# Optimization experiments

Measured on AMD Instinct MI355X. Metric: run time of the kernel, lower is better.

Reference implementation:

```python
import jax, jax.numpy as jnp
import numpy as np
import math

B, N = 1, 512
C_S, C_Z, C_H, H, PQ, PV = 384, 128, 16, 12, 4, 8
INF, EPS = 100000.0, 1e-8


def setup_inputs() -> dict:
    key = jax.random.key(0)
    ks = jax.random.split(key, 16)
    sc = 0.02
    return {
        "s": jax.random.normal(ks[0], (B, N, C_S), jnp.float32),
        "z": jax.random.normal(ks[1], (B, N, N, C_Z), jnp.float32),
        "t_trans": jax.random.normal(ks[2], (B, N, 3), jnp.float32),
        "t_rots": jax.random.normal(ks[3], (B, N, 3, 3), jnp.float32),
        "mask": jnp.ones((B, N), jnp.float32),
        "Wq": jax.random.normal(ks[4], (C_S, H * C_H), jnp.float32) * sc,
        "bq": jnp.zeros((H * C_H,), jnp.float32),
        "Wkv": jax.random.normal(ks[5], (C_S, 2 * H * C_H), jnp.float32) * sc,
        "bkv": jnp.zeros((2 * H * C_H,), jnp.float32),
        "Wqp": jax.random.normal(ks[6], (C_S, H * PQ * 3), jnp.float32) * sc,
        "bqp": jnp.zeros((H * PQ * 3,), jnp.float32),
        "Wkvp": jax.random.normal(ks[7], (C_S, H * (PQ + PV) * 3), jnp.float32) * sc,
        "bkvp": jnp.zeros((H * (PQ + PV) * 3,), jnp.float32),
        "Wb": jax.random.normal(ks[8], (C_Z, H), jnp.float32) * sc,
        "bb": jnp.zeros((H,), jnp.float32),
        "head_weights": jnp.full((H,), 0.5413, jnp.float32),  # softplus^-1(1) init
        "Wout": jax.random.normal(ks[9], (H * (C_Z + C_H + PV * 4), C_S), jnp.float32) * sc,
        "bout": jnp.zeros((C_S,), jnp.float32),
    }


def _split3_stack(x):
    # torch.split into 3 chunks along -1, then stack on new last axis -> [..., P, 3]
    return jnp.stack(jnp.split(x, 3, axis=-1), axis=-1)


def reference(s, z, t_trans, t_rots, mask, Wq, bq, Wkv, bkv, Wqp, bqp, Wkvp, bkvp,
              Wb, bb, head_weights, Wout, bout):
    q = (s @ Wq + bq).reshape(B, N, H, C_H)
    kv = (s @ Wkv + bkv).reshape(B, N, H, 2 * C_H)
    k, v = kv[..., :C_H], kv[..., C_H:]

    # point projections, moved to global frame: r @ p + t
    qp = _split3_stack(s @ Wqp + bqp)                      # [B,N,H*PQ,3] local
    qp = jnp.einsum('bnij,bnpj->bnpi', t_rots, qp) + t_trans[:, :, None, :]
    q_pts = qp.reshape(B, N, H, PQ, 3)
    kvp = _split3_stack(s @ Wkvp + bkvp)                   # [B,N,H*(PQ+PV),3]
    kvp = jnp.einsum('bnij,bnpj->bnpi', t_rots, kvp) + t_trans[:, :, None, :]
    kvp = kvp.reshape(B, N, H, PQ + PV, 3)
    k_pts, v_pts = kvp[..., :PQ, :], kvp[..., PQ:, :]

    b = z @ Wb + bb                                        # [B,N,N,H]

    a = jnp.einsum('bihc,bjhc->bhij', q, k) * math.sqrt(1.0 / (3 * C_H))
    a = a + math.sqrt(1.0 / 3) * jnp.transpose(b, (0, 3, 1, 2))

    # point-distance attention: [B,N,N,H,PQ]
    d2 = jnp.sum((q_pts[:, :, None] - k_pts[:, None]) ** 2, axis=-1)
    hw = jax.nn.softplus(head_weights) * math.sqrt(1.0 / (3 * (PQ * 9.0 / 2)))
    a = a + (-0.5) * jnp.einsum('bijhp,h->bhij', d2, hw)

    square_mask = INF * (mask[:, :, None] * mask[:, None, :] - 1.0)  # [B,N,N]
    a = jax.nn.softmax(a + square_mask[:, None], axis=-1)  # [B,H,N,N]

    o = jnp.einsum('bhij,bjhc->bihc', a, v).reshape(B, N, H * C_H)

    o_pt = jnp.einsum('bhij,bjhpx->bihpx', a, v_pts)       # [B,N,H,PV,3] global
    # invert frame: r^T @ (p - t)
    o_pt = jnp.einsum('bnji,bnhpj->bnhpi', t_rots, o_pt - t_trans[:, :, None, None, :])
    o_pt_norm = jnp.sqrt(jnp.sum(o_pt ** 2, axis=-1) + EPS).reshape(B, N, H * PV)
    o_pt = o_pt.reshape(B, N, H * PV, 3)

    o_pair = jnp.einsum('bhij,bijc->bihc', a, z).reshape(B, N, H * C_Z)

    cat = jnp.concatenate(
        [o, o_pt[..., 0], o_pt[..., 1], o_pt[..., 2], o_pt_norm, o_pair], axis=-1)
    return cat @ Wout + bout
```

## Files before the change

### kernel.cpp

```cpp
#include <hip/hip_runtime.h>
#include <math.h>

#define N 512
#define CS 384
#define CZ 128
#define CH 16
#define NH 12
#define PQ 4
#define PV 8

#define OFF_Q     0
#define OFF_K     98304
#define OFF_QRAW  294912
#define OFF_KVRAW 368640
#define OFF_QPTS  589824
#define OFF_KPTS  663552
#define OFF_VPX   737280
#define OFF_VPY   786432
#define OFF_VPZ   835584
#define OFF_A     884736
#define OFF_CAT   4030464
#define OFF_VT    5111808
#define OFF_WBT   5210112

__global__ __launch_bounds__(384) void init_out_kernel(
    const float* __restrict__ bout, const float* __restrict__ Wb,
    float* __restrict__ out, float* __restrict__ ws)
{
    out[(size_t)blockIdx.x * 384 + threadIdx.x] = bout[threadIdx.x];
    if (blockIdx.x == 0) {
        for (int idx = threadIdx.x; idx < NH * CZ; idx += 384) {
            int h = idx >> 7, c = idx & 127;
            ws[OFF_WBT + idx] = Wb[c * NH + h];
        }
    }
}

__global__ __launch_bounds__(256) void proj_kernel(
    const float* __restrict__ s,
    const float* __restrict__ Wq,  const float* __restrict__ bq,
    const float* __restrict__ Wkv, const float* __restrict__ bkv,
    const float* __restrict__ Wqp, const float* __restrict__ bqp,
    const float* __restrict__ Wkvp,const float* __restrict__ bkvp,
    float* __restrict__ ws)
{
    __shared__ float st[16 * CS];
    const int n0 = blockIdx.x * 16;
    for (int idx = threadIdx.x * 4; idx < 16 * CS; idx += 1024)
        *(float4*)&st[idx] = *(const float4*)&s[n0 * CS + idx];
    __syncthreads();

    const int tc = threadIdx.x & 31;
    const int tr = threadIdx.x >> 5;
    const int u0 = blockIdx.y * 128 + tc * 4;
    const int r0 = tr * 2;

    const float* W; const float* bptr; int ncol, lc0;
    if (u0 < 192)      { W = Wq;   bptr = bq;   ncol = 192; lc0 = u0; }
    else if (u0 < 576) { W = Wkv;  bptr = bkv;  ncol = 384; lc0 = u0 - 192; }
    else if (u0 < 720) { W = Wqp;  bptr = bqp;  ncol = 144; lc0 = u0 - 576; }
    else               { W = Wkvp; bptr = bkvp; ncol = 432; lc0 = u0 - 720; }

    float acc[2][4];
    #pragma unroll
    for (int r = 0; r < 2; r++)
        #pragma unroll
        for (int c = 0; c < 4; c++) acc[r][c] = 0.f;

    for (int k = 0; k < CS; k += 4) {
        float4 w0 = *(const float4*)&W[(k + 0) * ncol + lc0];
        float4 w1 = *(const float4*)&W[(k + 1) * ncol + lc0];
        float4 w2 = *(const float4*)&W[(k + 2) * ncol + lc0];
        float4 w3 = *(const float4*)&W[(k + 3) * ncol + lc0];
        #pragma unroll
        for (int r = 0; r < 2; r++) {
            float4 sv = *(const float4*)&st[(r0 + r) * CS + k];
            acc[r][0] += sv.x * w0.x + sv.y * w1.x + sv.z * w2.x + sv.w * w3.x;
            acc[r][1] += sv.x * w0.y + sv.y * w1.y + sv.z * w2.y + sv.w * w3.y;
            acc[r][2] += sv.x * w0.z + sv.y * w1.z + sv.z * w2.z + sv.w * w3.z;
            acc[r][3] += sv.x * w0.w + sv.y * w1.w + sv.z * w2.w + sv.w * w3.w;
        }
    }

    #pragma unroll
    for (int c = 0; c < 4; c++) {
        const int u = u0 + c;
        const float bias = bptr[lc0 + c];
        #pragma unroll
        for (int r = 0; r < 2; r++) {
            const int n = n0 + r0 + r;
            int oidx;
            if (u < 192) oidx = OFF_Q + n * 192 + u;
            else if (u < 576) {
                int lc = u - 192, h = lc >> 5, w = lc & 31;
                oidx = (w < 16) ? OFF_K + n * 192 + h * 16 + w
                                : OFF_VT + (h * 16 + (w - 16)) * 512 + n;
            } else if (u < 720) oidx = OFF_QRAW + n * 144 + (u - 576);
            else                oidx = OFF_KVRAW + n * 432 + (u - 720);
            ws[oidx] = acc[r][c] + bias;
        }
    }
}

__global__ __launch_bounds__(192) void point_kernel(
    const float* __restrict__ t_trans, const float* __restrict__ t_rots,
    float* __restrict__ ws)
{
    const int n = blockIdx.x;
    const int t = threadIdx.x;
    __shared__ float R[9], tr[3];
    if (t < 9) R[t] = t_rots[n * 9 + t];
    if (t < 3) tr[t] = t_trans[n * 3 + t];
    __syncthreads();

    float x0, x1, x2;
    if (t < 48) {
        int idx = t;
        x0 = ws[OFF_QRAW + n * 144 + 0 * 48 + idx];
        x1 = ws[OFF_QRAW + n * 144 + 1 * 48 + idx];
        x2 = ws[OFF_QRAW + n * 144 + 2 * 48 + idx];
        int h = idx >> 2, p = idx & 3;
        int base = OFF_QPTS + ((n * NH + h) * PQ + p) * 3;
        ws[base + 0] = R[0] * x0 + R[1] * x1 + R[2] * x2 + tr[0];
        ws[base + 1] = R[3] * x0 + R[4] * x1 + R[5] * x2 + tr[1];
        ws[base + 2] = R[6] * x0 + R[7] * x1 + R[8] * x2 + tr[2];
    } else if (t < 192) {
        int idx = t - 48;
        x0 = ws[OFF_KVRAW + n * 432 + 0 * 144 + idx];
        x1 = ws[OFF_KVRAW + n * 432 + 1 * 144 + idx];
        x2 = ws[OFF_KVRAW + n * 432 + 2 * 144 + idx];
        int h = idx / 12, p = idx % 12;
        float rx = R[0] * x0 + R[1] * x1 + R[2] * x2 + tr[0];
        float ry = R[3] * x0 + R[4] * x1 + R[5] * x2 + tr[1];
        float rz = R[6] * x0 + R[7] * x1 + R[8] * x2 + tr[2];
        if (p < PQ) {
            int base = OFF_KPTS + ((n * NH + h) * PQ + p) * 3;
            ws[base + 0] = rx; ws[base + 1] = ry; ws[base + 2] = rz;
        } else {
            int e = h * PV + (p - PQ);
            ws[OFF_VPX + e * 512 + n] = rx;
            ws[OFF_VPY + e * 512 + n] = ry;
            ws[OFF_VPZ + e * 512 + n] = rz;
        }
    }
}

__global__ __launch_bounds__(192) void logitA_kernel(
    const float* __restrict__ mask, const float* __restrict__ hweights,
    float* __restrict__ ws)
{
    const int j0 = blockIdx.x * 16;
    const int i0 = blockIdx.y * 16;
    const int t = threadIdx.x;

    __shared__ float qt[16 * 200];
    __shared__ float kt[16 * 200];
    __shared__ float qpt[16 * 148];
    __shared__ float kpt[16 * 148];
    __shared__ float mi[16], mj[16];

    {
        const float* src = ws + OFF_Q + i0 * 192;
        for (int idx = t * 4; idx < 3072; idx += 768)
            *(float4*)&qt[(idx / 192) * 200 + idx % 192] = *(const float4*)&src[idx];
    }
    {
        const float* src = ws + OFF_K + j0 * 192;
        for (int idx = t * 4; idx < 3072; idx += 768)
            *(float4*)&kt[(idx / 192) * 200 + idx % 192] = *(const float4*)&src[idx];
    }
    {
        const float* src = ws + OFF_QPTS + i0 * 144;
        for (int idx = t * 4; idx < 2304; idx += 768)
            *(float4*)&qpt[(idx / 144) * 148 + idx % 144] = *(const float4*)&src[idx];
    }
    {
        const float* src = ws + OFF_KPTS + j0 * 144;
        for (int idx = t * 4; idx < 2304; idx += 768)
            *(float4*)&kpt[(idx / 144) * 148 + idx % 144] = *(const float4*)&src[idx];
    }
    if (t < 16) { mi[t] = mask[i0 + t]; mj[t] = mask[j0 + t]; }
    __syncthreads();

    const int jj = t & 15;
    const int h = t >> 4;
    const float hw = log1pf(expf(hweights[h])) * 0.13608276348795434f;
    const float cqk = 0.14433756729740643f;

    float4 kr0 = *(const float4*)&kt[jj * 200 + h * 16 + 0];
    float4 kr1 = *(const float4*)&kt[jj * 200 + h * 16 + 4];
    float4 kr2 = *(const float4*)&kt[jj * 200 + h * 16 + 8];
    float4 kr3 = *(const float4*)&kt[jj * 200 + h * 16 + 12];
    float4 kp0 = *(const float4*)&kpt[jj * 148 + h * 12 + 0];
    float4 kp1 = *(const float4*)&kpt[jj * 148 + h * 12 + 4];
    float4 kp2 = *(const float4*)&kpt[jj * 148 + h * 12 + 8];
    const float mjv = mj[jj];

    for (int ii = 0; ii < 16; ii++) {
        float4 q0 = *(const float4*)&qt[ii * 200 + h * 16 + 0];
        float4 q1 = *(const float4*)&qt[ii * 200 + h * 16 + 4];
        float4 q2 = *(const float4*)&qt[ii * 200 + h * 16 + 8];
        float4 q3 = *(const float4*)&qt[ii * 200 + h * 16 + 12];
        float qk = q0.x * kr0.x + q0.y * kr0.y + q0.z * kr0.z + q0.w * kr0.w
                 + q1.x * kr1.x + q1.y * kr1.y + q1.z * kr1.z + q1.w * kr1.w
                 + q2.x * kr2.x + q2.y * kr2.y + q2.z * kr2.z + q2.w * kr2.w
                 + q3.x * kr3.x + q3.y * kr3.y + q3.z * kr3.z + q3.w * kr3.w;
        float4 p0 = *(const float4*)&qpt[ii * 148 + h * 12 + 0];
        float4 p1 = *(const float4*)&qpt[ii * 148 + h * 12 + 4];
        float4 p2 = *(const float4*)&qpt[ii * 148 + h * 12 + 8];
        float e, d2 = 0.f;
        e = p0.x - kp0.x; d2 += e * e;  e = p0.y - kp0.y; d2 += e * e;
        e = p0.z - kp0.z; d2 += e * e;  e = p0.w - kp0.w; d2 += e * e;
        e = p1.x - kp1.x; d2 += e * e;  e = p1.y - kp1.y; d2 += e * e;
        e = p1.z - kp1.z; d2 += e * e;  e = p1.w - kp1.w; d2 += e * e;
        e = p2.x - kp2.x; d2 += e * e;  e = p2.y - kp2.y; d2 += e * e;
        e = p2.z - kp2.z; d2 += e * e;  e = p2.w - kp2.w; d2 += e * e;
        float sm = 100000.0f * (mi[ii] * mjv - 1.0f);
        ws[OFF_A + ((size_t)(i0 + ii) * NH + h) * N + j0 + jj] =
            qk * cqk - 0.5f * hw * d2 + sm;
    }
}

__global__ __launch_bounds__(512) void bsoft_kernel(
    const float* __restrict__ z, const float* __restrict__ bb,
    float* ws)
{
    const int i = blockIdx.x;
    const int t = threadIdx.x;
    __shared__ float zt[128 * 132];
    __shared__ float wred[8][4];

    const int jj = t & 127;
    const int hg = __builtin_amdgcn_readfirstlane(t >> 7);
    const int h0 = hg * 3;
    const float bb0 = bb[h0], bb1 = bb[h0 + 1], bb2 = bb[h0 + 2];
    const float cb = 0.5773502691896258f;
    const float* w0 = ws + OFF_WBT + (h0 + 0) * 128;
    const float* w1 = ws + OFF_WBT + (h0 + 1) * 128;
    const float* w2 = ws + OFF_WBT + (h0 + 2) * 128;

    float lg[3][4];

    for (int T = 0; T < 4; T++) {
        __syncthreads();
        const float* zsrc = z + ((size_t)i * N + T * 128) * CZ;
        for (int idx = t * 4; idx < 16384; idx += 2048)
            *(float4*)&zt[(idx >> 7) * 132 + (idx & 127)] = *(const float4*)&zsrc[idx];
        __syncthreads();

        float a0 = bb0, a1 = bb1, a2 = bb2;
        const float* zr = &zt[jj * 132];
        #pragma unroll
        for (int c = 0; c < CZ; c += 4) {
            float4 zq = *(const float4*)&zr[c];
            float4 q0 = *(const float4*)&w0[c];
            float4 q1 = *(const float4*)&w1[c];
            float4 q2 = *(const float4*)&w2[c];
            a0 += zq.x * q0.x + zq.y * q0.y + zq.z * q0.z + zq.w * q0.w;
            a1 += zq.x * q1.x + zq.y * q1.y + zq.z * q1.z + zq.w * q1.w;
            a2 += zq.x * q2.x + zq.y * q2.y + zq.z * q2.z + zq.w * q2.w;
        }
        const float* arow = ws + OFF_A + (size_t)i * NH * N + T * 128 + jj;
        lg[0][T] = arow[(size_t)(h0 + 0) * N] + cb * a0;
        lg[1][T] = arow[(size_t)(h0 + 1) * N] + cb * a1;
        lg[2][T] = arow[(size_t)(h0 + 2) * N] + cb * a2;
    }

    const int wv = t >> 6;
    float mx[3], sm[3];
    #pragma unroll
    for (int r = 0; r < 3; r++) {
        float m = fmaxf(fmaxf(lg[r][0], lg[r][1]), fmaxf(lg[r][2], lg[r][3]));
        #pragma unroll
        for (int o = 32; o > 0; o >>= 1) m = fmaxf(m, __shfl_xor(m, o));
        mx[r] = m;
    }
    if ((t & 63) == 0) { wred[wv][0] = mx[0]; wred[wv][1] = mx[1]; wred[wv][2] = mx[2]; }
    __syncthreads();
    #pragma unroll
    for (int r = 0; r < 3; r++)
        mx[r] = fmaxf(wred[hg * 2][r], wred[hg * 2 + 1][r]);
    __syncthreads();
    #pragma unroll
    for (int r = 0; r < 3; r++) {
        float s = 0.f;
        #pragma unroll
        for (int T = 0; T < 4; T++) { lg[r][T] = __expf(lg[r][T] - mx[r]); s += lg[r][T]; }
        #pragma unroll
        for (int o = 32; o > 0; o >>= 1) s += __shfl_xor(s, o);
        sm[r] = s;
    }
    if ((t & 63) == 0) { wred[wv][0] = sm[0]; wred[wv][1] = sm[1]; wred[wv][2] = sm[2]; }
    __syncthreads();
    #pragma unroll
    for (int r = 0; r < 3; r++) {
        float inv = 1.0f / (wred[hg * 2][r] + wred[hg * 2 + 1][r]);
        float* prow = ws + OFF_A + ((size_t)i * NH + h0 + r) * N + jj;
        #pragma unroll
        for (int T = 0; T < 4; T++)
            prow[T * 128] = lg[r][T] * inv;
    }
}

__global__ __launch_bounds__(576) void finish_kernel(
    const float* __restrict__ z, const float* __restrict__ t_trans,
    const float* __restrict__ t_rots, const float* __restrict__ ws_c,
    float* __restrict__ ws)
{
    const int i = blockIdx.x;
    const int t = threadIdx.x;
    __shared__ float a_s[12 * 520];
    __shared__ float red[48 * 128];

    {
        const float* src = ws_c + OFF_A + (size_t)i * (NH * N);
        for (int idx = t * 4; idx < NH * N; idx += 576 * 4) {
            float4 v = *(const float4*)&src[idx];
            *(float4*)&a_s[(idx >> 9) * 520 + (idx & 511)] = v;
        }
    }
    __syncthreads();

    float* cat = ws + OFF_CAT + (size_t)i * 2112;
    const int wave = t >> 6;
    const int lane = t & 63;

    if (wave < 4) {
        const int c0 = 2 * lane;
        float acc[12][2];
        #pragma unroll
        for (int h = 0; h < 12; h++) { acc[h][0] = 0.f; acc[h][1] = 0.f; }
        const float* zbase = z + ((size_t)i * N + wave * 128) * CZ + c0;
        const int jb = wave * 128;
        for (int j0 = 0; j0 < 128; j0 += 4) {
            float2 z0 = *(const float2*)&zbase[(size_t)(j0 + 0) * CZ];
            float2 z1 = *(const float2*)&zbase[(size_t)(j0 + 1) * CZ];
            float2 z2 = *(const float2*)&zbase[(size_t)(j0 + 2) * CZ];
            float2 z3 = *(const float2*)&zbase[(size_t)(j0 + 3) * CZ];
            #pragma unroll
            for (int h = 0; h < 12; h++) {
                float4 p = *(const float4*)&a_s[h * 520 + jb + j0];
                acc[h][0] += p.x * z0.x + p.y * z1.x + p.z * z2.x + p.w * z3.x;
                acc[h][1] += p.x * z0.y + p.y * z1.y + p.z * z2.y + p.w * z3.y;
            }
        }
        #pragma unroll
        for (int h = 0; h < 12; h++)
            *(float2*)&red[(wave * 12 + h) * 128 + c0] = make_float2(acc[h][0], acc[h][1]);
    } else if (wave < 7) {
        const int u = t - 256, h = u >> 4, cc = u & 15;
        const float* vt = ws_c + OFF_VT + (h * 16 + cc) * 512;
        const float* ah = a_s + h * 520;
        float acc = 0.f;
        for (int j = 0; j < N; j += 4) {
            float4 av = *(const float4*)&ah[j];
            float4 vv = *(const float4*)&vt[j];
            acc += av.x * vv.x + av.y * vv.y + av.z * vv.z + av.w * vv.w;
        }
        cat[h * 16 + cc] = acc;
    } else if (t < 544) {
        const int u = t - 448, h = u >> 3;
        const float* vx = ws_c + OFF_VPX + u * 512;
        const float* vy = ws_c + OFF_VPY + u * 512;
        const float* vz = ws_c + OFF_VPZ + u * 512;
        const float* ah = a_s + h * 520;
        float g0 = 0.f, g1 = 0.f, g2 = 0.f;
        for (int j = 0; j < N; j += 4) {
            float4 av = *(const float4*)&ah[j];
            float4 x4 = *(const float4*)&vx[j];
            float4 y4 = *(const float4*)&vy[j];
            float4 z4 = *(const float4*)&vz[j];
            g0 += av.x * x4.x + av.y * x4.y + av.z * x4.z + av.w * x4.w;
            g1 += av.x * y4.x + av.y * y4.y + av.z * y4.z + av.w * y4.w;
            g2 += av.x * z4.x + av.y * z4.y + av.z * z4.z + av.w * z4.w;
        }
        float R[9], ti[3];
        #pragma unroll
        for (int x = 0; x < 9; x++) R[x] = t_rots[i * 9 + x];
        #pragma unroll
        for (int x = 0; x < 3; x++) ti[x] = t_trans[i * 3 + x];
        g0 -= ti[0]; g1 -= ti[1]; g2 -= ti[2];
        float l0 = R[0] * g0 + R[3] * g1 + R[6] * g2;
        float l1 = R[1] * g0 + R[4] * g1 + R[7] * g2;
        float l2 = R[2] * g0 + R[5] * g1 + R[8] * g2;
        float nrm = sqrtf(l0 * l0 + l1 * l1 + l2 * l2 + 1e-8f);
        cat[192 + u] = l0;
        cat[288 + u] = l1;
        cat[384 + u] = l2;
        cat[480 + u] = nrm;
    }
    __syncthreads();
    if (t < 512) {
        const int c = t & 127, hg = t >> 7;
        #pragma unroll
        for (int r = 0; r < 3; r++) {
            int h = hg * 3 + r;
            float v = red[(0 * 12 + h) * 128 + c] + red[(1 * 12 + h) * 128 + c]
                    + red[(2 * 12 + h) * 128 + c] + red[(3 * 12 + h) * 128 + c];
            cat[576 + h * CZ + c] = v;
        }
    }
}

__global__ __launch_bounds__(384) void out_kernel(
    const float* __restrict__ Wout, const float* __restrict__ ws,
    float* __restrict__ out)
{
    const int rt = blockIdx.x;
    const int kc = blockIdx.y;
    const int t = threadIdx.x;
    __shared__ float ct[8 * 264];
    for (int idx = t * 4; idx < 8 * 264; idx += 1536) {
        int rr = idx / 264, kk = idx % 264;
        *(float4*)&ct[idx] =
            *(const float4*)&ws[OFF_CAT + (size_t)(rt * 8 + rr) * 2112 + kc * 264 + kk];
    }
    __syncthreads();
    const int cq = t % 96, rg = t / 96;
    const int c0 = cq * 4;
    float acc[2][4] = {};
    const float* Wp = Wout + (size_t)kc * 264 * 384 + c0;
    for (int kk = 0; kk < 264; kk++) {
        float4 w = *(const float4*)&Wp[(size_t)kk * 384];
        float s0 = ct[(rg * 2 + 0) * 264 + kk];
        float s1 = ct[(rg * 2 + 1) * 264 + kk];
        acc[0][0] += s0 * w.x; acc[0][1] += s0 * w.y; acc[0][2] += s0 * w.z; acc[0][3] += s0 * w.w;
        acc[1][0] += s1 * w.x; acc[1][1] += s1 * w.y; acc[1][2] += s1 * w.z; acc[1][3] += s1 * w.w;
    }
    #pragma unroll
    for (int r = 0; r < 2; r++) {
        float* op = out + (size_t)(rt * 8 + rg * 2 + r) * 384 + c0;
        atomicAdd(&op[0], acc[r][0]);
        atomicAdd(&op[1], acc[r][1]);
        atomicAdd(&op[2], acc[r][2]);
        atomicAdd(&op[3], acc[r][3]);
    }
}

extern "C" void kernel_launch(void* const* d_in, const int* in_sizes, int n_in,
                              void* d_out, int out_size, void* d_ws, size_t ws_size,
                              hipStream_t stream) {
    const float* s       = (const float*)d_in[0];
    const float* z       = (const float*)d_in[1];
    const float* t_trans = (const float*)d_in[2];
    const float* t_rots  = (const float*)d_in[3];
    const float* mask    = (const float*)d_in[4];
    const float* Wq      = (const float*)d_in[5];
    const float* bq      = (const float*)d_in[6];
    const float* Wkv     = (const float*)d_in[7];
    const float* bkv     = (const float*)d_in[8];
    const float* Wqp     = (const float*)d_in[9];
    const float* bqp     = (const float*)d_in[10];
    const float* Wkvp    = (const float*)d_in[11];
    const float* bkvp    = (const float*)d_in[12];
    const float* Wb      = (const float*)d_in[13];
    const float* bb      = (const float*)d_in[14];
    const float* hweights= (const float*)d_in[15];
    const float* Wout    = (const float*)d_in[16];
    const float* bout    = (const float*)d_in[17];
    float* ws  = (float*)d_ws;
    float* out = (float*)d_out;

    init_out_kernel<<<512, 384, 0, stream>>>(bout, Wb, out, ws);
    proj_kernel<<<dim3(32, 9), 256, 0, stream>>>(s, Wq, bq, Wkv, bkv, Wqp, bqp, Wkvp, bkvp, ws);
    point_kernel<<<512, 192, 0, stream>>>(t_trans, t_rots, ws);
    logitA_kernel<<<dim3(32, 32), 192, 0, stream>>>(mask, hweights, ws);
    bsoft_kernel<<<512, 512, 0, stream>>>(z, bb, ws);
    finish_kernel<<<512, 576, 0, stream>>>(z, t_trans, t_rots, ws, ws);
    out_kernel<<<dim3(64, 8), 384, 0, stream>>>(Wout, ws, out);
}
```

Before: 438.5 us.

## Restructure bias-softmax, pair-attention and output GEMM for more register reuse

bsoft_kernel now runs 256 threads with 6 heads per thread and stages the Wb transpose in shared memory. finish_kernel stages z tiles through shared memory, and 128 threads each accumulate 4 channels by 6 heads, with one cross-group reduction replacing the previous 4-wave split over direct global reads. out_kernel splits K four ways per block so each thread computes all 8 rows, then reduces in shared memory before the atomics. The aim is fewer redundant global and shared loads, at the cost of fewer active threads for the z·a product and lower occupancy.

```diff
diff --git a/kernel.cpp b/kernel.cpp
--- a/kernel.cpp
+++ b/kernel.cpp
@@ -221,68 +221,77 @@
     }
 }
 
-__global__ __launch_bounds__(512) void bsoft_kernel(
+__global__ __launch_bounds__(256) void bsoft_kernel(
     const float* __restrict__ z, const float* __restrict__ bb,
-    float* ws)
+    float* __restrict__ ws)
 {
     const int i = blockIdx.x;
     const int t = threadIdx.x;
     __shared__ float zt[128 * 132];
-    __shared__ float wred[8][4];
+    __shared__ float wbt_s[12 * 132];
+    __shared__ float wred[4][6];
+
+    for (int idx = t; idx < NH * CZ; idx += 256) {
+        int h = idx >> 7, c = idx & 127;
+        wbt_s[h * 132 + c] = ws[OFF_WBT + idx];
+    }
 
     const int jj = t & 127;
     const int hg = __builtin_amdgcn_readfirstlane(t >> 7);
-    const int h0 = hg * 3;
-    const float bb0 = bb[h0], bb1 = bb[h0 + 1], bb2 = bb[h0 + 2];
+    const int h0 = hg * 6;
+    float bias[6];
+    #pragma unroll
+    for (int r = 0; r < 6; r++) bias[r] = bb[h0 + r];
     const float cb = 0.5773502691896258f;
-    const float* w0 = ws + OFF_WBT + (h0 + 0) * 128;
-    const float* w1 = ws + OFF_WBT + (h0 + 1) * 128;
-    const float* w2 = ws + OFF_WBT + (h0 + 2) * 128;
-
-    float lg[3][4];
+
+    float lg[6][4];
 
     for (int T = 0; T < 4; T++) {
         __syncthreads();
         const float* zsrc = z + ((size_t)i * N + T * 128) * CZ;
-        for (int idx = t * 4; idx < 16384; idx += 2048)
+        for (int idx = t * 4; idx < 16384; idx += 1024)
             *(float4*)&zt[(idx >> 7) * 132 + (idx & 127)] = *(const float4*)&zsrc[idx];
         __syncthreads();
 
-        float a0 = bb0, a1 = bb1, a2 = bb2;
+        float a[6];
+        #pragma unroll
+        for (int r = 0; r < 6; r++) a[r] = bias[r];
         const float* zr = &zt[jj * 132];
-        #pragma unroll
+        #pragma unroll 8
         for (int c = 0; c < CZ; c += 4) {
             float4 zq = *(const float4*)&zr[c];
-            float4 q0 = *(const float4*)&w0[c];
-            float4 q1 = *(const float4*)&w1[c];
-            float4 q2 = *(const float4*)&w2[c];
-            a0 += zq.x * q0.x + zq.y * q0.y + zq.z * q0.z + zq.w * q0.w;
-            a1 += zq.x * q1.x + zq.y * q1.y + zq.z * q1.z + zq.w * q1.w;
-            a2 += zq.x * q2.x + zq.y * q2.y + zq.z * q2.z + zq.w * q2.w;
+            #pragma unroll
+            for (int r = 0; r < 6; r++) {
+                float4 wq = *(const float4*)&wbt_s[(h0 + r) * 132 + c];
+                a[r] += zq.x * wq.x + zq.y * wq.y + zq.z * wq.z + zq.w * wq.w;
+            }
         }
         const float* arow = ws + OFF_A + (size_t)i * NH * N + T * 128 + jj;
-        lg[0][T] = arow[(size_t)(h0 + 0) * N] + cb * a0;
-        lg[1][T] = arow[(size_t)(h0 + 1) * N] + cb * a1;
-        lg[2][T] = arow[(size_t)(h0 + 2) * N] + cb * a2;
+        #pragma unroll
+        for (int r = 0; r < 6; r++)
+            lg[r][T] = arow[(size_t)(h0 + r) * N] + cb * a[r];
     }
 
     const int wv = t >> 6;
-    float mx[3], sm[3];
-    #pragma unroll
-    for (int r = 0; r < 3; r++) {
+    float mx[6];
+    #pragma unroll
+    for (int r = 0; r < 6; r++) {
         float m = fmaxf(fmaxf(lg[r][0], lg[r][1]), fmaxf(lg[r][2], lg[r][3]));
         #pragma unroll
         for (int o = 32; o > 0; o >>= 1) m = fmaxf(m, __shfl_xor(m, o));
         mx[r] = m;
     }
-    if ((t & 63) == 0) { wred[wv][0] = mx[0]; wred[wv][1] = mx[1]; wred[wv][2] = mx[2]; }
-    __syncthreads();
-    #pragma unroll
-    for (int r = 0; r < 3; r++)
+    if ((t & 63) == 0)
+        #pragma unroll
+        for (int r = 0; r < 6; r++) wred[wv][r] = mx[r];
+    __syncthreads();
+    #pragma unroll
+    for (int r = 0; r < 6; r++)
         mx[r] = fmaxf(wred[hg * 2][r], wred[hg * 2 + 1][r]);
     __syncthreads();
-    #pragma unroll
-    for (int r = 0; r < 3; r++) {
+    float sm[6];
+    #pragma unroll
+    for (int r = 0; r < 6; r++) {
         float s = 0.f;
         #pragma unroll
         for (int T = 0; T < 4; T++) { lg[r][T] = __expf(lg[r][T] - mx[r]); s += lg[r][T]; }
@@ -290,10 +299,12 @@
         for (int o = 32; o > 0; o >>= 1) s += __shfl_xor(s, o);
         sm[r] = s;
     }
-    if ((t & 63) == 0) { wred[wv][0] = sm[0]; wred[wv][1] = sm[1]; wred[wv][2] = sm[2]; }
-    __syncthreads();
-    #pragma unroll
-    for (int r = 0; r < 3; r++) {
+    if ((t & 63) == 0)
+        #pragma unroll
+        for (int r = 0; r < 6; r++) wred[wv][r] = sm[r];
+    __syncthreads();
+    #pragma unroll
+    for (int r = 0; r < 6; r++) {
         float inv = 1.0f / (wred[hg * 2][r] + wred[hg * 2 + 1][r]);
         float* prow = ws + OFF_A + ((size_t)i * NH + h0 + r) * N + jj;
         #pragma unroll
@@ -302,7 +313,7 @@
     }
 }
 
-__global__ __launch_bounds__(576) void finish_kernel(
+__global__ __launch_bounds__(512) void finish_kernel(
     const float* __restrict__ z, const float* __restrict__ t_trans,
     const float* __restrict__ t_rots, const float* __restrict__ ws_c,
     float* __restrict__ ws)
@@ -310,11 +321,12 @@
     const int i = blockIdx.x;
     const int t = threadIdx.x;
     __shared__ float a_s[12 * 520];
-    __shared__ float red[48 * 128];
+    __shared__ float zt[64 * 132];
+    __shared__ float red2[64 * 24];
 
     {
         const float* src = ws_c + OFF_A + (size_t)i * (NH * N);
-        for (int idx = t * 4; idx < NH * N; idx += 576 * 4) {
+        for (int idx = t * 4; idx < NH * N; idx += 2048) {
             float4 v = *(const float4*)&src[idx];
             *(float4*)&a_s[(idx >> 9) * 520 + (idx & 511)] = v;
         }
@@ -322,49 +334,27 @@
     __syncthreads();
 
     float* cat = ws + OFF_CAT + (size_t)i * 2112;
-    const int wave = t >> 6;
-    const int lane = t & 63;
-
-    if (wave < 4) {
-        const int c0 = 2 * lane;
-        float acc[12][2];
-        #pragma unroll
-        for (int h = 0; h < 12; h++) { acc[h][0] = 0.f; acc[h][1] = 0.f; }
-        const float* zbase = z + ((size_t)i * N + wave * 128) * CZ + c0;
-        const int jb = wave * 128;
-        for (int j0 = 0; j0 < 128; j0 += 4) {
-            float2 z0 = *(const float2*)&zbase[(size_t)(j0 + 0) * CZ];
-            float2 z1 = *(const float2*)&zbase[(size_t)(j0 + 1) * CZ];
-            float2 z2 = *(const float2*)&zbase[(size_t)(j0 + 2) * CZ];
-            float2 z3 = *(const float2*)&zbase[(size_t)(j0 + 3) * CZ];
-            #pragma unroll
-            for (int h = 0; h < 12; h++) {
-                float4 p = *(const float4*)&a_s[h * 520 + jb + j0];
-                acc[h][0] += p.x * z0.x + p.y * z1.x + p.z * z2.x + p.w * z3.x;
-                acc[h][1] += p.x * z0.y + p.y * z1.y + p.z * z2.y + p.w * z3.y;
-            }
-        }
-        #pragma unroll
-        for (int h = 0; h < 12; h++)
-            *(float2*)&red[(wave * 12 + h) * 128 + c0] = make_float2(acc[h][0], acc[h][1]);
-    } else if (wave < 7) {
-        const int u = t - 256, h = u >> 4, cc = u & 15;
-        const float* vt = ws_c + OFF_VT + (h * 16 + cc) * 512;
+
+    if (t < 192) {
+        const int h = t >> 4;
+        const float* vt = ws_c + OFF_VT + t * 512;
         const float* ah = a_s + h * 520;
         float acc = 0.f;
+        #pragma unroll 4
         for (int j = 0; j < N; j += 4) {
             float4 av = *(const float4*)&ah[j];
             float4 vv = *(const float4*)&vt[j];
             acc += av.x * vv.x + av.y * vv.y + av.z * vv.z + av.w * vv.w;
         }
-        cat[h * 16 + cc] = acc;
-    } else if (t < 544) {
-        const int u = t - 448, h = u >> 3;
+        cat[t] = acc;
+    } else if (t < 288) {
+        const int u = t - 192, h = u >> 3;
         const float* vx = ws_c + OFF_VPX + u * 512;
         const float* vy = ws_c + OFF_VPY + u * 512;
         const float* vz = ws_c + OFF_VPZ + u * 512;
         const float* ah = a_s + h * 520;
         float g0 = 0.f, g1 = 0.f, g2 = 0.f;
+        #pragma unroll 2
         for (int j = 0; j < N; j += 4) {
             float4 av = *(const float4*)&ah[j];
             float4 x4 = *(const float4*)&vx[j];
@@ -389,15 +379,57 @@
         cat[384 + u] = l2;
         cat[480 + u] = nrm;
     }
-    __syncthreads();
-    if (t < 512) {
-        const int c = t & 127, hg = t >> 7;
-        #pragma unroll
-        for (int r = 0; r < 3; r++) {
-            int h = hg * 3 + r;
-            float v = red[(0 * 12 + h) * 128 + c] + red[(1 * 12 + h) * 128 + c]
-                    + red[(2 * 12 + h) * 128 + c] + red[(3 * 12 + h) * 128 + c];
-            cat[576 + h * CZ + c] = v;
+
+    const int q  = t & 31;
+    const int hg = (t >> 5) & 1;
+    const int jg = t >> 6;
+    const int c0 = q * 4;
+    const int h0 = hg * 6;
+    float4 acc[6];
+    #pragma unroll
+    for (int r = 0; r < 6; r++) acc[r] = make_float4(0.f, 0.f, 0.f, 0.f);
+
+    for (int T = 0; T < 8; T++) {
+        __syncthreads();
+        const float* zsrc = z + ((size_t)i * N + T * 64) * CZ;
+        for (int idx = t * 4; idx < 8192; idx += 2048) {
+            float4 v = *(const float4*)&zsrc[idx];
+            *(float4*)&zt[(idx >> 7) * 132 + (idx & 127)] = v;
+        }
+        __syncthreads();
+        if (t < 128) {
+            const int jb = T * 64 + jg * 32;
+            const int jl = jg * 32;
+            #pragma unroll 4
+            for (int j0 = 0; j0 < 32; j0 += 4) {
+                float4 z0 = *(const float4*)&zt[(jl + j0 + 0) * 132 + c0];
+                float4 z1 = *(const float4*)&zt[(jl + j0 + 1) * 132 + c0];
+                float4 z2 = *(const float4*)&zt[(jl + j0 + 2) * 132 + c0];
+                float4 z3 = *(const float4*)&zt[(jl + j0 + 3) * 132 + c0];
+                #pragma unroll
+                for (int r = 0; r < 6; r++) {
+                    float4 a = *(const float4*)&a_s[(h0 + r) * 520 + jb + j0];
+                    acc[r].x += a.x * z0.x + a.y * z1.x + a.z * z2.x + a.w * z3.x;
+                    acc[r].y += a.x * z0.y + a.y * z1.y + a.z * z2.y + a.w * z3.y;
+                    acc[r].z += a.x * z0.z + a.y * z1.z + a.z * z2.z + a.w * z3.z;
+                    acc[r].w += a.x * z0.w + a.y * z1.w + a.z * z2.w + a.w * z3.w;
+                }
+            }
+        }
+    }
+    if (t >= 64 && t < 128) {
+        #pragma unroll
+        for (int r = 0; r < 6; r++)
+            *(float4*)&red2[(t - 64) * 24 + r * 4] = acc[r];
+    }
+    __syncthreads();
+    if (t < 64) {
+        #pragma unroll
+        for (int r = 0; r < 6; r++) {
+            float4 p = *(const float4*)&red2[t * 24 + r * 4];
+            float4 v = make_float4(acc[r].x + p.x, acc[r].y + p.y,
+                                   acc[r].z + p.z, acc[r].w + p.w);
+            *(float4*)&cat[576 + (h0 + r) * CZ + c0] = v;
         }
     }
 }
@@ -410,30 +442,46 @@
     const int kc = blockIdx.y;
     const int t = threadIdx.x;
     __shared__ float ct[8 * 264];
+    __shared__ float red[32 * 384];
     for (int idx = t * 4; idx < 8 * 264; idx += 1536) {
         int rr = idx / 264, kk = idx % 264;
         *(float4*)&ct[idx] =
             *(const float4*)&ws[OFF_CAT + (size_t)(rt * 8 + rr) * 2112 + kc * 264 + kk];
     }
     __syncthreads();
-    const int cq = t % 96, rg = t / 96;
+    const int cq = t % 96, kg = t / 96;
     const int c0 = cq * 4;
-    float acc[2][4] = {};
-    const float* Wp = Wout + (size_t)kc * 264 * 384 + c0;
-    for (int kk = 0; kk < 264; kk++) {
+    float4 acc[8];
+    #pragma unroll
+    for (int r = 0; r < 8; r++) acc[r] = make_float4(0.f, 0.f, 0.f, 0.f);
+    const float* Wp = Wout + ((size_t)kc * 264 + kg * 66) * 384 + c0;
+    const float* cp = ct + kg * 66;
+    for (int kk = 0; kk < 66; kk++) {
         float4 w = *(const float4*)&Wp[(size_t)kk * 384];
-        float s0 = ct[(rg * 2 + 0) * 264 + kk];
-        float s1 = ct[(rg * 2 + 1) * 264 + kk];
-        acc[0][0] += s0 * w.x; acc[0][1] += s0 * w.y; acc[0][2] += s0 * w.z; acc[0][3] += s0 * w.w;
-        acc[1][0] += s1 * w.x; acc[1][1] += s1 * w.y; acc[1][2] += s1 * w.z; acc[1][3] += s1 * w.w;
-    }
-    #pragma unroll
-    for (int r = 0; r < 2; r++) {
-        float* op = out + (size_t)(rt * 8 + rg * 2 + r) * 384 + c0;
-        atomicAdd(&op[0], acc[r][0]);
-        atomicAdd(&op[1], acc[r][1]);
-        atomicAdd(&op[2], acc[r][2]);
-        atomicAdd(&op[3], acc[r][3]);
+        #pragma unroll
+        for (int r = 0; r < 8; r++) {
+            float sv = cp[r * 264 + kk];
+            acc[r].x += sv * w.x; acc[r].y += sv * w.y;
+            acc[r].z += sv * w.z; acc[r].w += sv * w.w;
+        }
+    }
+    #pragma unroll
+    for (int r = 0; r < 8; r++)
+        *(float4*)&red[(kg * 8 + r) * 384 + c0] = acc[r];
+    __syncthreads();
+    #pragma unroll
+    for (int g = 0; g < 2; g++) {
+        int lin = t * 4 + g * 1536;
+        int r = lin / 384, c = lin % 384;
+        float4 v0 = *(const float4*)&red[(0 * 8 + r) * 384 + c];
+        float4 v1 = *(const float4*)&red[(1 * 8 + r) * 384 + c];
+        float4 v2 = *(const float4*)&red[(2 * 8 + r) * 384 + c];
+        float4 v3 = *(const float4*)&red[(3 * 8 + r) * 384 + c];
+        float* op = out + (size_t)(rt * 8 + r) * 384 + c;
+        atomicAdd(&op[0], v0.x + v1.x + v2.x + v3.x);
+        atomicAdd(&op[1], v0.y + v1.y + v2.y + v3.y);
+        atomicAdd(&op[2], v0.z + v1.z + v2.z + v3.z);
+        atomicAdd(&op[3], v0.w + v1.w + v2.w + v3.w);
     }
 }
 
@@ -465,7 +513,7 @@
     proj_kernel<<<dim3(32, 9), 256, 0, stream>>>(s, Wq, bq, Wkv, bkv, Wqp, bqp, Wkvp, bkvp, ws);
     point_kernel<<<512, 192, 0, stream>>>(t_trans, t_rots, ws);
     logitA_kernel<<<dim3(32, 32), 192, 0, stream>>>(mask, hweights, ws);
-    bsoft_kernel<<<512, 512, 0, stream>>>(z, bb, ws);
-    finish_kernel<<<512, 576, 0, stream>>>(z, t_trans, t_rots, ws, ws);
+    bsoft_kernel<<<512, 256, 0, stream>>>(z, bb, ws);
+    finish_kernel<<<512, 512, 0, stream>>>(z, t_trans, t_rots, ws, ws);
     out_kernel<<<dim3(64, 8), 384, 0, stream>>>(Wout, ws, out);
 }
```

Measured after the change: 520.8 us. 1.19x slower.
